# Optimization experiments

Hardware: AMD Instinct MI355X
Metric: run time of the kernel (lower is better)

Reference implementation:

```python
import jax, jax.numpy as jnp
import numpy as np

D, H, DFF = 1024, 16, 4096
HD = D // H
NEG = -1e9  # finite stand-in for -inf causal mask (grad-safe)


def layer_norm(x, g, b, eps=1e-5):
    mu = jnp.mean(x, axis=-1, keepdims=True)
    var = jnp.mean(jnp.square(x - mu), axis=-1, keepdims=True)
    return (x - mu) * jax.lax.rsqrt(var + eps) * g + b


def setup_inputs() -> dict:
    key = jax.random.key(0)
    ks = jax.random.split(key, 16)
    B, T = 2, 2048
    x = jax.random.normal(ks[0], (B, T, D), jnp.float32)
    causal_mask = jnp.where(jnp.triu(jnp.ones((T, T), bool), k=1), NEG, 0.0).astype(jnp.float32)
    ema_attn = jax.random.uniform(ks[1], (H, T, T), jnp.float32)
    # normalize EMA rows like attention weights would be
    ema_attn = ema_attn / jnp.sum(ema_attn, axis=-1, keepdims=True)
    s = 0.02
    p = {
        'x': x, 'causal_mask': causal_mask, 'ema_attn': ema_attn,
        'log_tau_attn': jnp.array(0.0, jnp.float32),
        'Wq': jax.random.normal(ks[2], (D, D), jnp.float32) * s,
        'bq': jnp.zeros((D,), jnp.float32),
        'Wk': jax.random.normal(ks[3], (D, D), jnp.float32) * s,
        'bk': jnp.zeros((D,), jnp.float32),
        'Wv': jax.random.normal(ks[4], (D, D), jnp.float32) * s,
        'bv': jnp.zeros((D,), jnp.float32),
        'Wo': jax.random.normal(ks[5], (D, D), jnp.float32) * s,
        'bo': jnp.zeros((D,), jnp.float32),
        'W1': jax.random.normal(ks[6], (DFF, D), jnp.float32) * s,
        'b1': jnp.zeros((DFF,), jnp.float32),
        'W2': jax.random.normal(ks[7], (D, DFF), jnp.float32) * s,
        'b2': jnp.zeros((D,), jnp.float32),
        'g1': jnp.ones((D,), jnp.float32), 'beta1': jnp.zeros((D,), jnp.float32),
        'g2': jnp.ones((D,), jnp.float32), 'beta2': jnp.zeros((D,), jnp.float32),
    }
    return p


def reference(x, causal_mask, ema_attn, log_tau_attn, Wq, bq, Wk, bk, Wv, bv,
              Wo, bo, W1, b1, W2, b2, g1, beta1, g2, beta2):
    B, T, _ = x.shape
    # habituation bias: -tau_a * mean over heads of the EMA attention
    tau_a = jnp.exp(log_tau_attn)
    habit_bias = -(tau_a * ema_attn).mean(0)            # (T, T)
    attn_mask = causal_mask + habit_bias                # (T, T)

    # multi-head self-attention (torch MHA math, dropout=0 / eval)
    q = (x @ Wq.T + bq).reshape(B, T, H, HD)
    k = (x @ Wk.T + bk).reshape(B, T, H, HD)
    v = (x @ Wv.T + bv).reshape(B, T, H, HD)
    scores = jnp.einsum('bthd,bshd->bhts', q, k) / jnp.sqrt(jnp.float32(HD))
    scores = scores + attn_mask[None, None]             # (B, H, T, T)
    attn = jax.nn.softmax(scores, axis=-1)
    ctx = jnp.einsum('bhts,bshd->bthd', attn, v).reshape(B, T, D)
    attn_out = ctx @ Wo.T + bo

    # residual + norm, then FFN (GELU), residual + norm
    h = layer_norm(x + attn_out, g1, beta1)
    ff = (jax.nn.gelu(h @ W1.T + b1) @ W2.T) + b2
    out = layer_norm(h + ff, g2, beta2)
    return out
```

## Files before the change

### kernel.cpp

```cpp
#include <hip/hip_runtime.h>
#include <hip/hip_bf16.h>
#include <math.h>

#define T_SEQ 2048
#define D_MODEL 1024
#define BT 4096

typedef __bf16 bf16;
typedef __bf16 bf16x8 __attribute__((ext_vector_type(8)));
typedef __bf16 bf16x4 __attribute__((ext_vector_type(4)));
typedef float f32x4 __attribute__((ext_vector_type(4)));

__device__ __forceinline__ void gload_lds16(const bf16* g, bf16* l) {
  __builtin_amdgcn_global_load_lds(
      (__attribute__((address_space(1))) void*)(g),
      (__attribute__((address_space(3))) void*)(l), 16, 0, 0);
}

__global__ __launch_bounds__(256) void k_mask(const float* __restrict__ causal,
                                              const float* __restrict__ ema,
                                              const float* __restrict__ logtau,
                                              bf16* __restrict__ mask) {
  const int qt = blockIdx.x, st = blockIdx.y;
  if (st > qt) return;
  const int t = threadIdx.x;
  const float c = -__expf(logtau[0]) * (1.0f / 16.0f);
  const int r0 = t >> 4;
  const int cc = t & 15;
#pragma unroll
  for (int rr = 0; rr < 4; ++rr) {
    const size_t q = (size_t)qt * 64 + r0 + rr * 16;
    const size_t f4 = q * 512 + st * 16 + cc;
    float4 v = ((const float4*)causal)[f4];
    float a0 = v.x, a1 = v.y, a2 = v.z, a3 = v.w;
#pragma unroll
    for (int h = 0; h < 16; ++h) {
      float4 e = ((const float4*)(ema + (size_t)h * T_SEQ * T_SEQ))[f4];
      a0 += c * e.x; a1 += c * e.y; a2 += c * e.z; a3 += c * e.w;
    }
    bf16x4 o;
    o[0] = (bf16)a0; o[1] = (bf16)a1; o[2] = (bf16)a2; o[3] = (bf16)a3;
    ((bf16x4*)mask)[f4] = o;
  }
}

struct CvtArgs {
  const float* src[7];
  bf16* dst[7];
  int cum[8];
};
__global__ __launch_bounds__(256) void k_cvt_all(CvtArgs a) {
  const int i = blockIdx.x * 256 + threadIdx.x;
  if (i >= a.cum[7]) return;
  int s = 0;
#pragma unroll
  for (int k = 1; k < 7; ++k) s += (i >= a.cum[k]);
  const int j = i - a.cum[s];
  float4 v = ((const float4*)a.src[s])[j];
  bf16x4 o;
  o[0] = (bf16)v.x; o[1] = (bf16)v.y; o[2] = (bf16)v.z; o[3] = (bf16)v.w;
  ((bf16x4*)a.dst[s])[j] = o;
}

__global__ void k_bias3(const float* __restrict__ bq, const float* __restrict__ bk,
                        const float* __restrict__ bv, float* __restrict__ o) {
  const int i = blockIdx.x * 256 + threadIdx.x;
  o[i] = (i < 1024) ? bq[i] : (i < 2048 ? bk[i - 1024] : bv[i - 2048]);
}

__device__ __forceinline__ float gelu_tanh(float x) {
  return 0.5f * x * (1.0f + tanhf(0.7978845608028654f * (x + 0.044715f * x * x * x)));
}

template <int EPI>
__global__ __launch_bounds__(512, 2) void k_gemm_big(const bf16* __restrict__ A,
                                                     const bf16* __restrict__ B,
                                                     const float* __restrict__ bias,
                                                     const float* __restrict__ resid,
                                                     float* __restrict__ outf,
                                                     bf16* __restrict__ outb,
                                                     int K, int N) {
  __shared__ bf16 sA[2][256 * 64];
  __shared__ bf16 sB[2][256 * 64];
  const int tid = threadIdx.x;
  const int m0 = blockIdx.x * 256, n0 = blockIdx.y * 256;
  const int lane = tid & 63;
  const int w = tid >> 6, wr = w >> 2, wc = w & 3;
  const int lr = lane & 15, lg = lane >> 4;

  const int srow = lane >> 3;
  const int schunk = (lane & 7) ^ srow;

  auto stage = [&](int buf, int kt) {
    const int k0 = kt << 6;
#pragma unroll
    for (int e = 0; e < 4; ++e) {
      const int r = w * 32 + e * 8 + srow;
      gload_lds16(A + (size_t)(m0 + r) * K + k0 + schunk * 8,
                  &sA[buf][(w * 32 + e * 8) * 64 + lane * 8]);
      gload_lds16(B + (size_t)(n0 + r) * K + k0 + schunk * 8,
                  &sB[buf][(w * 32 + e * 8) * 64 + lane * 8]);
    }
  };

  f32x4 acc[8][4] = {};

  stage(0, 0);
  stage(1, 1);

  const int KT = K >> 6;
  for (int t = 0; t < KT; ++t) {
    if (t < KT - 1) asm volatile("s_waitcnt vmcnt(8)" ::: "memory");
    else            asm volatile("s_waitcnt vmcnt(0)" ::: "memory");
    __builtin_amdgcn_s_barrier();

    const int buf = t & 1;
    const char* pA = (const char*)sA[buf];
    const char* pB = (const char*)sB[buf];

    bf16x8 a0[8], b0[4];
#pragma unroll
    for (int m = 0; m < 8; ++m) {
      const int row = wr * 128 + m * 16 + lr;
      a0[m] = *(const bf16x8*)(pA + (unsigned)(row * 128) +
                               (((unsigned)lg) ^ (unsigned)(row & 7)) * 16u);
    }
#pragma unroll
    for (int n = 0; n < 4; ++n) {
      const int row = wc * 64 + n * 16 + lr;
      b0[n] = *(const bf16x8*)(pB + (unsigned)(row * 128) +
                               (((unsigned)lg) ^ (unsigned)(row & 7)) * 16u);
    }
    __builtin_amdgcn_s_setprio(1);
#pragma unroll
    for (int m = 0; m < 8; ++m)
#pragma unroll
      for (int n = 0; n < 4; ++n)
        acc[m][n] = __builtin_amdgcn_mfma_f32_16x16x32_bf16(a0[m], b0[n], acc[m][n], 0, 0, 0);
    __builtin_amdgcn_s_setprio(0);

    bf16x8 a1[8], b1[4];
#pragma unroll
    for (int m = 0; m < 8; ++m) {
      const int row = wr * 128 + m * 16 + lr;
      a1[m] = *(const bf16x8*)(pA + (unsigned)(row * 128) +
                               (((unsigned)(4 | lg)) ^ (unsigned)(row & 7)) * 16u);
    }
#pragma unroll
    for (int n = 0; n < 4; ++n) {
      const int row = wc * 64 + n * 16 + lr;
      b1[n] = *(const bf16x8*)(pB + (unsigned)(row * 128) +
                               (((unsigned)(4 | lg)) ^ (unsigned)(row & 7)) * 16u);
    }
    asm volatile("s_waitcnt lgkmcnt(0)" ::: "memory");
    __builtin_amdgcn_s_barrier();
    if (t + 2 < KT) stage(buf, t + 2);

    __builtin_amdgcn_s_setprio(1);
#pragma unroll
    for (int m = 0; m < 8; ++m)
#pragma unroll
      for (int n = 0; n < 4; ++n)
        acc[m][n] = __builtin_amdgcn_mfma_f32_16x16x32_bf16(a1[m], b1[n], acc[m][n], 0, 0, 0);
    __builtin_amdgcn_s_setprio(0);
  }

  const int row0 = m0 + wr * 128 + (lane >> 4) * 4;
  const int col0 = n0 + wc * 64 + lr;
#pragma unroll
  for (int m = 0; m < 8; ++m) {
#pragma unroll
    for (int n = 0; n < 4; ++n) {
      const int col = col0 + n * 16;
      const float bv = bias[col];
#pragma unroll
      for (int r = 0; r < 4; ++r) {
        const int row = row0 + m * 16 + r;
        float v = acc[m][n][r] + bv;
        if (EPI == 0) {
          outb[(size_t)row * N + col] = (bf16)v;
        } else if (EPI == 1) {
          v += resid[(size_t)row * N + col];
          outf[(size_t)row * N + col] = v;
        } else {
          outb[(size_t)row * N + col] = (bf16)gelu_tanh(v);
        }
      }
    }
  }
}

__global__ __launch_bounds__(256, 2) void k_gemm_splitk(const bf16* __restrict__ A,
                                                        const bf16* __restrict__ B,
                                                        const float* __restrict__ bias,
                                                        float* __restrict__ p0,
                                                        float* __restrict__ p1,
                                                        int K, int N, int Kc) {
  __shared__ bf16 sA[2][128 * 64];
  __shared__ bf16 sB[2][128 * 64];
  const int tid = threadIdx.x;
  const int m0 = blockIdx.x * 128, n0 = blockIdx.y * 128;
  const int z = blockIdx.z;
  const int kb = z * Kc;
  float* __restrict__ po = z ? p1 : p0;
  const int lane = tid & 63;
  const int w = tid >> 6, wr = w >> 1, wc = w & 1;
  const int lr = lane & 15, lg = lane >> 4;

  const int srow = lane >> 3;
  const int schunk = (lane & 7) ^ srow;

  auto stage = [&](int buf, int kt) {
    const int k0 = kb + (kt << 6);
#pragma unroll
    for (int e = 0; e < 4; ++e) {
      const int r = w * 32 + e * 8 + srow;
      gload_lds16(A + (size_t)(m0 + r) * K + k0 + schunk * 8,
                  &sA[buf][(w * 32 + e * 8) * 64 + lane * 8]);
      gload_lds16(B + (size_t)(n0 + r) * K + k0 + schunk * 8,
                  &sB[buf][(w * 32 + e * 8) * 64 + lane * 8]);
    }
  };

  f32x4 acc[4][4] = {};

  stage(0, 0);
  stage(1, 1);

  const int KT = Kc >> 6;
  for (int t = 0; t < KT; ++t) {
    if (t < KT - 1) asm volatile("s_waitcnt vmcnt(8)" ::: "memory");
    else            asm volatile("s_waitcnt vmcnt(0)" ::: "memory");
    __builtin_amdgcn_s_barrier();

    const int buf = t & 1;
    const char* pA = (const char*)sA[buf];
    const char* pB = (const char*)sB[buf];
    bf16x8 af[4][2], bfr[4][2];
#pragma unroll
    for (int m = 0; m < 4; ++m) {
      const int row = wr * 64 + m * 16 + lr;
#pragma unroll
      for (int kk = 0; kk < 2; ++kk) {
        const unsigned off =
            (unsigned)(row * 128) + (((unsigned)((kk << 2) | lg)) ^ (unsigned)(row & 7)) * 16u;
        af[m][kk] = *(const bf16x8*)(pA + off);
      }
    }
#pragma unroll
    for (int n = 0; n < 4; ++n) {
      const int row = wc * 64 + n * 16 + lr;
#pragma unroll
      for (int kk = 0; kk < 2; ++kk) {
        const unsigned off =
            (unsigned)(row * 128) + (((unsigned)((kk << 2) | lg)) ^ (unsigned)(row & 7)) * 16u;
        bfr[n][kk] = *(const bf16x8*)(pB + off);
      }
    }
    asm volatile("s_waitcnt lgkmcnt(0)" ::: "memory");
    __builtin_amdgcn_s_barrier();
    if (t + 2 < KT) stage(buf, t + 2);

    __builtin_amdgcn_s_setprio(1);
#pragma unroll
    for (int m = 0; m < 4; ++m)
#pragma unroll
      for (int n = 0; n < 4; ++n)
#pragma unroll
        for (int kk = 0; kk < 2; ++kk)
          acc[m][n] = __builtin_amdgcn_mfma_f32_16x16x32_bf16(af[m][kk], bfr[n][kk],
                                                              acc[m][n], 0, 0, 0);
    __builtin_amdgcn_s_setprio(0);
  }

  const int row0 = m0 + wr * 64 + (lane >> 4) * 4;
  const int col0 = n0 + wc * 64 + lr;
#pragma unroll
  for (int m = 0; m < 4; ++m) {
#pragma unroll
    for (int n = 0; n < 4; ++n) {
      const int col = col0 + n * 16;
      const float bv = z ? 0.0f : bias[col];
#pragma unroll
      for (int r = 0; r < 4; ++r) {
        const int row = row0 + m * 16 + r;
        po[(size_t)row * N + col] = acc[m][n][r] + bv;
      }
    }
  }
}

__global__ __launch_bounds__(256, 3) void k_attn(const bf16* __restrict__ qkv,
                                                 const bf16* __restrict__ maskb,
                                                 bf16* __restrict__ ctx) {
  const int bh = blockIdx.x;
  const int qt = blockIdx.y;
  const int b = bh >> 4, h = bh & 15;
  const int tid = threadIdx.x, w = tid >> 6, lane = tid & 63;
  const int lr = lane & 15, lg = lane >> 4;

  __shared__ bf16 sK[2][64 * 64];
  __shared__ bf16 sVt[2][64 * 72];
  __shared__ bf16 sP[4][16 * 64];

  const size_t rs = 3072;
  const bf16* base = qkv + (size_t)b * T_SEQ * rs + h * 64;
  const int q0b = qt * 64;
  const int qrow = w * 16 + lr;
  const bf16* mrow = maskb + (size_t)(q0b + qrow) * T_SEQ;

  bf16x8 qf[2];
#pragma unroll
  for (int kk = 0; kk < 2; ++kk) {
    bf16x8 q = *(const bf16x8*)(base + (size_t)(q0b + qrow) * rs + kk * 32 + lg * 8);
#pragma unroll
    for (int j = 0; j < 8; ++j) qf[kk][j] = (bf16)((float)q[j] * 0.125f);
  }

  const int srow = lane >> 3;
  const int scol = lane & 7;

  auto issueK = [&](int s0, bf16* sKb) {
#pragma unroll
    for (int e = 0; e < 2; ++e) {
      const int kb = w * 16 + e * 8;
      const int r = kb + srow;
      const int cs = 8 * (scol ^ (r & 7));
      gload_lds16(base + (size_t)(s0 + r) * rs + 1024 + cs, &sKb[kb * 64 + lane * 8]);
    }
  };
  auto loadV = [&](int s0, bf16x8 vv[2]) {
#pragma unroll
    for (int t = 0; t < 2; ++t) {
      const int c = w * 64 + lane + t * 256;
      vv[t] = *(const bf16x8*)(base + (size_t)(s0 + (c >> 3)) * rs + 2048 + (c & 7) * 8);
    }
  };
  auto writeV = [&](const bf16x8 vv[2], bf16* sVtb) {
    char* pb = (char*)sVtb;
#pragma unroll
    for (int t = 0; t < 2; ++t) {
      const int c = w * 64 + lane + t * 256;
      const int s = c >> 3, dc = c & 7;
#pragma unroll
      for (int j = 0; j < 8; ++j) {
        const unsigned ba = ((unsigned)((dc * 8 + j) * 72 + s) * 2) ^ ((unsigned)dc << 4);
        *(bf16*)(pb + ba) = vv[t][j];
      }
    }
  };

  float m_r = -3.0e38f, l_r = 0.0f;
  f32x4 o[4] = {};

  const float L2E = 1.44269504088896f;
  const int nt = qt + 1;
  const unsigned swzq = (unsigned)(lr & 7) << 4;

  {
    bf16x8 v0[2];
    loadV(0, v0);
    issueK(0, sK[0]);
    writeV(v0, sVt[0]);
  }
  __syncthreads();

  int cur = 0;
  for (int t = 0; t < nt; ++t, cur ^= 1) {
    const bool pf = (t + 1 < nt);
    bf16x8 vv[2];
    if (pf) {
      loadV((t + 1) * 64, vv);
      issueK((t + 1) * 64, sK[cur ^ 1]);
    }

    bf16x4 mk[4];
#pragma unroll
    for (int n = 0; n < 4; ++n)
      mk[n] = *(const bf16x4*)(mrow + t * 64 + n * 16 + lg * 4);

    const char* sKc = (const char*)sK[cur];
    f32x4 sc[4] = {};
    __builtin_amdgcn_s_setprio(1);
#pragma unroll
    for (int n = 0; n < 4; ++n) {
      const int key = n * 16 + lr;
#pragma unroll
      for (int kk = 0; kk < 2; ++kk) {
        const unsigned boff =
            (unsigned)(key * 128 + kk * 64 + lg * 16) ^ ((unsigned)(key & 7) << 4);
        bf16x8 kf = *(const bf16x8*)(sKc + boff);
        sc[n] = __builtin_amdgcn_mfma_f32_16x16x32_bf16(kf, qf[kk], sc[n], 0, 0, 0);
      }
    }
    __builtin_amdgcn_s_setprio(0);

    float mx = -3.0e38f;
#pragma unroll
    for (int n = 0; n < 4; ++n)
#pragma unroll
      for (int j = 0; j < 4; ++j) {
        sc[n][j] += (float)mk[n][j];
        mx = fmaxf(mx, sc[n][j]);
      }
    mx = fmaxf(mx, __shfl_xor(mx, 16));
    mx = fmaxf(mx, __shfl_xor(mx, 32));

    if (!__all(mx <= m_r + 8.0f)) {
      const float mnew = fmaxf(m_r, mx);
      const float alpha = exp2f((m_r - mnew) * L2E);
      m_r = mnew;
      l_r *= alpha;
      float a4[4];
#pragma unroll
      for (int j = 0; j < 4; ++j) a4[j] = __shfl(alpha, (lane & 48) | (lg * 4 + j));
#pragma unroll
      for (int dt = 0; dt < 4; ++dt)
#pragma unroll
        for (int j = 0; j < 4; ++j) o[dt][j] *= a4[j];
    }

    const float mL2 = m_r * L2E;
    float ps = 0.0f;
    float pn[4][4];
#pragma unroll
    for (int n = 0; n < 4; ++n)
#pragma unroll
      for (int j = 0; j < 4; ++j) {
        const float p = exp2f(sc[n][j] * L2E - mL2);
        pn[n][j] = p;
        ps += p;
      }
    ps += __shfl_xor(ps, 16);
    ps += __shfl_xor(ps, 32);
    l_r += ps;

    if (pf) writeV(vv, sVt[cur ^ 1]);

    char* sPw = (char*)sP[w];
#pragma unroll
    for (int n = 0; n < 4; ++n) {
      bf16x4 pb;
#pragma unroll
      for (int j = 0; j < 4; ++j) pb[j] = (bf16)pn[n][j];
      *(bf16x4*)(sPw + (((unsigned)(lr * 128 + n * 32 + lg * 8)) ^ swzq)) = pb;
    }

    bf16x8 pa[2];
#pragma unroll
    for (int kk = 0; kk < 2; ++kk)
      pa[kk] = *(const bf16x8*)(sPw + (((unsigned)(lr * 128 + kk * 64 + lg * 16)) ^ swzq));
    const char* sVc = (const char*)sVt[cur];
    __builtin_amdgcn_s_setprio(1);
#pragma unroll
    for (int dt = 0; dt < 4; ++dt) {
      const int dd = dt * 16 + lr;
#pragma unroll
      for (int kk = 0; kk < 2; ++kk) {
        const unsigned ba =
            ((unsigned)(dd * 72 + kk * 32 + lg * 8) * 2) ^ ((unsigned)((dd >> 3) & 7) << 4);
        bf16x8 vb = *(const bf16x8*)(sVc + ba);
        o[dt] = __builtin_amdgcn_mfma_f32_16x16x32_bf16(pa[kk], vb, o[dt], 0, 0, 0);
      }
    }
    __builtin_amdgcn_s_setprio(0);
    __syncthreads();
  }

  float linv[4];
#pragma unroll
  for (int j = 0; j < 4; ++j) linv[j] = 1.0f / __shfl(l_r, (lane & 48) | (lg * 4 + j));
#pragma unroll
  for (int j = 0; j < 4; ++j) {
    const size_t row = (size_t)b * T_SEQ + q0b + w * 16 + lg * 4 + j;
#pragma unroll
    for (int dt = 0; dt < 4; ++dt)
      ctx[row * D_MODEL + h * 64 + dt * 16 + lr] = (bf16)(o[dt][j] * linv[j]);
  }
}

__global__ __launch_bounds__(256) void k_ln3(const float* __restrict__ p0,
                                             const float* __restrict__ p1,
                                             const float* __restrict__ resid,
                                             const float* __restrict__ g,
                                             const float* __restrict__ be,
                                             float* __restrict__ out,
                                             bf16* __restrict__ outb) {
  const int row = blockIdx.x, tid = threadIdx.x;
  const size_t i4 = (size_t)row * 256 + tid;
  const float4 a = ((const float4*)p0)[i4];
  const float4 bq = ((const float4*)p1)[i4];
  const float4 cr = ((const float4*)resid)[i4];
  float4 v;
  v.x = a.x + bq.x + cr.x;
  v.y = a.y + bq.y + cr.y;
  v.z = a.z + bq.z + cr.z;
  v.w = a.w + bq.w + cr.w;
  float s = v.x + v.y + v.z + v.w;
  float s2 = v.x * v.x + v.y * v.y + v.z * v.z + v.w * v.w;
#pragma unroll
  for (int d = 1; d < 64; d <<= 1) { s += __shfl_xor(s, d); s2 += __shfl_xor(s2, d); }
  __shared__ float red[8];
  const int w = tid >> 6;
  if ((tid & 63) == 0) { red[w] = s; red[4 + w] = s2; }
  __syncthreads();
  s = red[0] + red[1] + red[2] + red[3];
  s2 = red[4] + red[5] + red[6] + red[7];
  const float mu = s * (1.0f / 1024.0f);
  const float var = s2 * (1.0f / 1024.0f) - mu * mu;
  const float inv = rsqrtf(var + 1e-5f);
  const int col = tid * 4;
  const float4 gv = *(const float4*)(g + col);
  const float4 bv = *(const float4*)(be + col);
  float4 y;
  y.x = (v.x - mu) * inv * gv.x + bv.x;
  y.y = (v.y - mu) * inv * gv.y + bv.y;
  y.z = (v.z - mu) * inv * gv.z + bv.z;
  y.w = (v.w - mu) * inv * gv.w + bv.w;
  *(float4*)(out + (size_t)row * 1024 + col) = y;
  if (outb) {
    bf16x4 ob;
    ob[0] = (bf16)y.x; ob[1] = (bf16)y.y; ob[2] = (bf16)y.z; ob[3] = (bf16)y.w;
    *(bf16x4*)(outb + (size_t)row * 1024 + col) = ob;
  }
}

extern "C" void kernel_launch(void* const* d_in, const int* in_sizes, int n_in,
                              void* d_out, int out_size, void* d_ws, size_t ws_size,
                              hipStream_t stream) {
  const float* x      = (const float*)d_in[0];
  const float* causal = (const float*)d_in[1];
  const float* ema    = (const float*)d_in[2];
  const float* logtau = (const float*)d_in[3];
  const float* Wq = (const float*)d_in[4];
  const float* bq = (const float*)d_in[5];
  const float* Wk = (const float*)d_in[6];
  const float* bk = (const float*)d_in[7];
  const float* Wv = (const float*)d_in[8];
  const float* bv = (const float*)d_in[9];
  const float* Wo = (const float*)d_in[10];
  const float* bo = (const float*)d_in[11];
  const float* W1 = (const float*)d_in[12];
  const float* b1 = (const float*)d_in[13];
  const float* W2 = (const float*)d_in[14];
  const float* b2 = (const float*)d_in[15];
  const float* g1  = (const float*)d_in[16];
  const float* be1 = (const float*)d_in[17];
  const float* g2  = (const float*)d_in[18];
  const float* be2 = (const float*)d_in[19];
  float* out = (float*)d_out;

  char* ws = (char*)d_ws;
  bf16*  maskb = (bf16*)(ws + 0);
  bf16*  x_bf  = (bf16*)(ws + (16UL << 20));
  bf16*  wqkv  = (bf16*)(ws + (24UL << 20));
  bf16*  wo_bf = (bf16*)(ws + (30UL << 20));
  bf16*  w1_bf = (bf16*)(ws + (32UL << 20));
  bf16*  w2_bf = (bf16*)(ws + (40UL << 20));
  float* bqkv  = (float*)(ws + (48UL << 20));
  bf16*  qkv   = (bf16*)(ws + (49UL << 20));
  bf16*  ctxb  = (bf16*)(ws + (73UL << 20));
  float* hbuf  = (float*)(ws + (97UL << 20));
  bf16*  h_bf  = (bf16*)(ws + (113UL << 20));
  bf16*  ff1   = (bf16*)(ws + (121UL << 20));
  float* part0 = (float*)(ws + (49UL << 20));
  float* part1 = (float*)(ws + 0);

  const dim3 blk(256);
  const dim3 blk512(512);

  k_mask<<<dim3(32, 32), blk, 0, stream>>>(causal, ema, logtau, maskb);

  CvtArgs ca;
  ca.src[0] = x;  ca.dst[0] = x_bf;
  ca.src[1] = Wq; ca.dst[1] = wqkv;
  ca.src[2] = Wk; ca.dst[2] = wqkv + (1UL << 20);
  ca.src[3] = Wv; ca.dst[3] = wqkv + (2UL << 20);
  ca.src[4] = Wo; ca.dst[4] = wo_bf;
  ca.src[5] = W1; ca.dst[5] = w1_bf;
  ca.src[6] = W2; ca.dst[6] = w2_bf;
  ca.cum[0] = 0;
  ca.cum[1] = 1048576;
  ca.cum[2] = 1048576 + 262144;
  ca.cum[3] = 1048576 + 524288;
  ca.cum[4] = 1048576 + 786432;
  ca.cum[5] = 2097152;
  ca.cum[6] = 2097152 + 1048576;
  ca.cum[7] = 4194304;
  k_cvt_all<<<dim3(16384), blk, 0, stream>>>(ca);
  k_bias3<<<dim3(12), blk, 0, stream>>>(bq, bk, bv, bqkv);

  k_gemm_big<0><<<dim3(16, 12), blk512, 0, stream>>>(x_bf, wqkv, bqkv, nullptr, nullptr,
                                                     qkv, 1024, 3072);

  k_attn<<<dim3(32, 32), blk, 0, stream>>>(qkv, maskb, ctxb);

  k_gemm_splitk<<<dim3(32, 8, 2), blk, 0, stream>>>(ctxb, wo_bf, bo, part0, part1,
                                                    1024, 1024, 512);

  k_ln3<<<dim3(4096), blk, 0, stream>>>(part0, part1, x, g1, be1, hbuf, h_bf);

  k_gemm_big<2><<<dim3(16, 16), blk512, 0, stream>>>(h_bf, w1_bf, b1, nullptr, nullptr,
                                                     ff1, 1024, 4096);

  k_gemm_splitk<<<dim3(32, 8, 2), blk, 0, stream>>>(ff1, w2_bf, b2, part0, part1,
                                                    4096, 1024, 2048);

  k_ln3<<<dim3(4096), blk, 0, stream>>>(part0, part1, hbuf, g2, be2, out, nullptr);
}
```

Measured before the change: 304.2 us.

## Widen attention blocks to 128 query rows with 8 waves sharing K/V tiles

The attention kernel now processes 128 query rows per block using 8 waves (512 threads), so each K/V tile loaded into LDS is shared by twice as many query rows. This halves the per-query K/V traffic and the block count. Blocks are also remapped so the y index pairs short and long causal rows, giving heavy tiles first. The mask kernel now fills one extra key tile beyond the diagonal, because the 128-row blocks walk a key range that extends past it. The costs are more LDS per block, lower occupancy, and a diagonal tile that does masked work.

```diff
diff --git a/kernel.cpp b/kernel.cpp
--- a/kernel.cpp
+++ b/kernel.cpp
@@ -22,7 +22,7 @@
                                               const float* __restrict__ logtau,
                                               bf16* __restrict__ mask) {
   const int qt = blockIdx.x, st = blockIdx.y;
-  if (st > qt) return;
+  if (st > qt + 1) return;
   const int t = threadIdx.x;
   const float c = -__expf(logtau[0]) * (1.0f / 16.0f);
   const int r0 = t >> 4;
@@ -290,22 +290,23 @@
   }
 }
 
-__global__ __launch_bounds__(256, 3) void k_attn(const bf16* __restrict__ qkv,
+__global__ __launch_bounds__(512, 4) void k_attn(const bf16* __restrict__ qkv,
                                                  const bf16* __restrict__ maskb,
                                                  bf16* __restrict__ ctx) {
   const int bh = blockIdx.x;
-  const int qt = blockIdx.y;
+  const int y = blockIdx.y;
+  const int qt2 = (y < 8) ? y : 23 - y;
   const int b = bh >> 4, h = bh & 15;
   const int tid = threadIdx.x, w = tid >> 6, lane = tid & 63;
   const int lr = lane & 15, lg = lane >> 4;
 
   __shared__ bf16 sK[2][64 * 64];
   __shared__ bf16 sVt[2][64 * 72];
-  __shared__ bf16 sP[4][16 * 64];
+  __shared__ bf16 sP[8][16 * 64];
 
   const size_t rs = 3072;
   const bf16* base = qkv + (size_t)b * T_SEQ * rs + h * 64;
-  const int q0b = qt * 64;
+  const int q0b = qt2 * 128;
   const int qrow = w * 16 + lr;
   const bf16* mrow = maskb + (size_t)(q0b + qrow) * T_SEQ;
 
@@ -321,32 +322,21 @@
   const int scol = lane & 7;
 
   auto issueK = [&](int s0, bf16* sKb) {
-#pragma unroll
-    for (int e = 0; e < 2; ++e) {
-      const int kb = w * 16 + e * 8;
-      const int r = kb + srow;
-      const int cs = 8 * (scol ^ (r & 7));
-      gload_lds16(base + (size_t)(s0 + r) * rs + 1024 + cs, &sKb[kb * 64 + lane * 8]);
-    }
+    const int kb = w * 8;
+    const int r = kb + srow;
+    const int cs = 8 * (scol ^ (r & 7));
+    gload_lds16(base + (size_t)(s0 + r) * rs + 1024 + cs, &sKb[kb * 64 + lane * 8]);
   };
-  auto loadV = [&](int s0, bf16x8 vv[2]) {
-#pragma unroll
-    for (int t = 0; t < 2; ++t) {
-      const int c = w * 64 + lane + t * 256;
-      vv[t] = *(const bf16x8*)(base + (size_t)(s0 + (c >> 3)) * rs + 2048 + (c & 7) * 8);
-    }
+  auto loadV = [&](int s0, bf16x8& vv) {
+    vv = *(const bf16x8*)(base + (size_t)(s0 + (tid >> 3)) * rs + 2048 + (tid & 7) * 8);
   };
-  auto writeV = [&](const bf16x8 vv[2], bf16* sVtb) {
+  auto writeV = [&](const bf16x8& vv, bf16* sVtb) {
     char* pb = (char*)sVtb;
-#pragma unroll
-    for (int t = 0; t < 2; ++t) {
-      const int c = w * 64 + lane + t * 256;
-      const int s = c >> 3, dc = c & 7;
-#pragma unroll
-      for (int j = 0; j < 8; ++j) {
-        const unsigned ba = ((unsigned)((dc * 8 + j) * 72 + s) * 2) ^ ((unsigned)dc << 4);
-        *(bf16*)(pb + ba) = vv[t][j];
-      }
+    const int s = tid >> 3, dc = tid & 7;
+#pragma unroll
+    for (int j = 0; j < 8; ++j) {
+      const unsigned ba = ((unsigned)((dc * 8 + j) * 72 + s) * 2) ^ ((unsigned)dc << 4);
+      *(bf16*)(pb + ba) = vv[j];
     }
   };
 
@@ -354,11 +344,11 @@
   f32x4 o[4] = {};
 
   const float L2E = 1.44269504088896f;
-  const int nt = qt + 1;
+  const int nt = 2 * qt2 + 2;
   const unsigned swzq = (unsigned)(lr & 7) << 4;
 
   {
-    bf16x8 v0[2];
+    bf16x8 v0;
     loadV(0, v0);
     issueK(0, sK[0]);
     writeV(v0, sVt[0]);
@@ -368,7 +358,7 @@
   int cur = 0;
   for (int t = 0; t < nt; ++t, cur ^= 1) {
     const bool pf = (t + 1 < nt);
-    bf16x8 vv[2];
+    bf16x8 vv;
     if (pf) {
       loadV((t + 1) * 64, vv);
       issueK((t + 1) * 64, sK[cur ^ 1]);
@@ -593,7 +583,7 @@
   k_gemm_big<0><<<dim3(16, 12), blk512, 0, stream>>>(x_bf, wqkv, bqkv, nullptr, nullptr,
                                                      qkv, 1024, 3072);
 
-  k_attn<<<dim3(32, 32), blk, 0, stream>>>(qkv, maskb, ctxb);
+  k_attn<<<dim3(32, 16), blk512, 0, stream>>>(qkv, maskb, ctxb);
 
   k_gemm_splitk<<<dim3(32, 8, 2), blk, 0, stream>>>(ctxb, wo_bf, bo, part0, part1,
                                                     1024, 1024, 512);
```

Measured after the change: 298.2 us. No clear change (-2.0%).

## Double attention query tile per block to reuse K/V tiles across two row groups

Applied to the files above, without the earlier changes.

Each attention block now covers 128 query rows instead of 64, with each wave handling two 16-row groups that share the same K and V fragments loaded from LDS. The query-tile index is remapped so heavy and light causal tiles are paired for load balance, and the mask kernel now fills one extra diagonal tile because key tiles extend past the 64-row diagonal. This halves K/V global and LDS traffic per query row and cuts the block count. In exchange it raises register use (occupancy hint lowered from 3 to 2) and gives fewer, longer blocks.

```diff
diff --git a/kernel.cpp b/kernel.cpp
--- a/kernel.cpp
+++ b/kernel.cpp
@@ -22,7 +22,7 @@
                                               const float* __restrict__ logtau,
                                               bf16* __restrict__ mask) {
   const int qt = blockIdx.x, st = blockIdx.y;
-  if (st > qt) return;
+  if (st > qt + 1) return;
   const int t = threadIdx.x;
   const float c = -__expf(logtau[0]) * (1.0f / 16.0f);
   const int r0 = t >> 4;
@@ -290,32 +290,36 @@
   }
 }
 
-__global__ __launch_bounds__(256, 3) void k_attn(const bf16* __restrict__ qkv,
+__global__ __launch_bounds__(256, 2) void k_attn(const bf16* __restrict__ qkv,
                                                  const bf16* __restrict__ maskb,
                                                  bf16* __restrict__ ctx) {
   const int bh = blockIdx.x;
-  const int qt = blockIdx.y;
+  const int y = blockIdx.y;
+  const int qt2 = (y < 8) ? y : 23 - y;
   const int b = bh >> 4, h = bh & 15;
   const int tid = threadIdx.x, w = tid >> 6, lane = tid & 63;
   const int lr = lane & 15, lg = lane >> 4;
 
   __shared__ bf16 sK[2][64 * 64];
   __shared__ bf16 sVt[2][64 * 72];
-  __shared__ bf16 sP[4][16 * 64];
+  __shared__ bf16 sP[4][32 * 64];
 
   const size_t rs = 3072;
   const bf16* base = qkv + (size_t)b * T_SEQ * rs + h * 64;
-  const int q0b = qt * 64;
-  const int qrow = w * 16 + lr;
-  const bf16* mrow = maskb + (size_t)(q0b + qrow) * T_SEQ;
-
-  bf16x8 qf[2];
-#pragma unroll
-  for (int kk = 0; kk < 2; ++kk) {
-    bf16x8 q = *(const bf16x8*)(base + (size_t)(q0b + qrow) * rs + kk * 32 + lg * 8);
-#pragma unroll
-    for (int j = 0; j < 8; ++j) qf[kk][j] = (bf16)((float)q[j] * 0.125f);
-  }
+  const int q0b = qt2 * 128;
+  const bf16* mrow0 = maskb + (size_t)(q0b + w * 32 + lr) * T_SEQ;
+  const bf16* mrow1 = mrow0 + (size_t)16 * T_SEQ;
+
+  bf16x8 qf[2][2];
+#pragma unroll
+  for (int qr = 0; qr < 2; ++qr)
+#pragma unroll
+    for (int kk = 0; kk < 2; ++kk) {
+      bf16x8 q = *(const bf16x8*)(base + (size_t)(q0b + w * 32 + qr * 16 + lr) * rs +
+                                  kk * 32 + lg * 8);
+#pragma unroll
+      for (int j = 0; j < 8; ++j) qf[qr][kk][j] = (bf16)((float)q[j] * 0.125f);
+    }
 
   const int srow = lane >> 3;
   const int scol = lane & 7;
@@ -350,11 +354,11 @@
     }
   };
 
-  float m_r = -3.0e38f, l_r = 0.0f;
-  f32x4 o[4] = {};
+  float m_r[2] = {-3.0e38f, -3.0e38f}, l_r[2] = {0.0f, 0.0f};
+  f32x4 o[2][4] = {};
 
   const float L2E = 1.44269504088896f;
-  const int nt = qt + 1;
+  const int nt = 2 * qt2 + 2;
   const unsigned swzq = (unsigned)(lr & 7) << 4;
 
   {
@@ -374,14 +378,15 @@
       issueK((t + 1) * 64, sK[cur ^ 1]);
     }
 
-    bf16x4 mk[4];
-#pragma unroll
-    for (int n = 0; n < 4; ++n)
-      mk[n] = *(const bf16x4*)(mrow + t * 64 + n * 16 + lg * 4);
+    bf16x4 mk[2][4];
+#pragma unroll
+    for (int n = 0; n < 4; ++n) {
+      mk[0][n] = *(const bf16x4*)(mrow0 + t * 64 + n * 16 + lg * 4);
+      mk[1][n] = *(const bf16x4*)(mrow1 + t * 64 + n * 16 + lg * 4);
+    }
 
     const char* sKc = (const char*)sK[cur];
-    f32x4 sc[4] = {};
-    __builtin_amdgcn_s_setprio(1);
+    bf16x8 kf[4][2];
 #pragma unroll
     for (int n = 0; n < 4; ++n) {
       const int key = n * 16 + lr;
@@ -389,69 +394,81 @@
       for (int kk = 0; kk < 2; ++kk) {
         const unsigned boff =
             (unsigned)(key * 128 + kk * 64 + lg * 16) ^ ((unsigned)(key & 7) << 4);
-        bf16x8 kf = *(const bf16x8*)(sKc + boff);
-        sc[n] = __builtin_amdgcn_mfma_f32_16x16x32_bf16(kf, qf[kk], sc[n], 0, 0, 0);
-      }
-    }
+        kf[n][kk] = *(const bf16x8*)(sKc + boff);
+      }
+    }
+
+    f32x4 sc[2][4] = {};
+    __builtin_amdgcn_s_setprio(1);
+#pragma unroll
+    for (int qr = 0; qr < 2; ++qr)
+#pragma unroll
+      for (int n = 0; n < 4; ++n)
+#pragma unroll
+        for (int kk = 0; kk < 2; ++kk)
+          sc[qr][n] = __builtin_amdgcn_mfma_f32_16x16x32_bf16(kf[n][kk], qf[qr][kk],
+                                                              sc[qr][n], 0, 0, 0);
     __builtin_amdgcn_s_setprio(0);
 
-    float mx = -3.0e38f;
-#pragma unroll
-    for (int n = 0; n < 4; ++n)
-#pragma unroll
-      for (int j = 0; j < 4; ++j) {
-        sc[n][j] += (float)mk[n][j];
-        mx = fmaxf(mx, sc[n][j]);
-      }
-    mx = fmaxf(mx, __shfl_xor(mx, 16));
-    mx = fmaxf(mx, __shfl_xor(mx, 32));
-
-    if (!__all(mx <= m_r + 8.0f)) {
-      const float mnew = fmaxf(m_r, mx);
-      const float alpha = exp2f((m_r - mnew) * L2E);
-      m_r = mnew;
-      l_r *= alpha;
-      float a4[4];
-#pragma unroll
-      for (int j = 0; j < 4; ++j) a4[j] = __shfl(alpha, (lane & 48) | (lg * 4 + j));
-#pragma unroll
-      for (int dt = 0; dt < 4; ++dt)
-#pragma unroll
-        for (int j = 0; j < 4; ++j) o[dt][j] *= a4[j];
-    }
-
-    const float mL2 = m_r * L2E;
-    float ps = 0.0f;
-    float pn[4][4];
-#pragma unroll
-    for (int n = 0; n < 4; ++n)
-#pragma unroll
-      for (int j = 0; j < 4; ++j) {
-        const float p = exp2f(sc[n][j] * L2E - mL2);
-        pn[n][j] = p;
-        ps += p;
-      }
-    ps += __shfl_xor(ps, 16);
-    ps += __shfl_xor(ps, 32);
-    l_r += ps;
+    float pn[2][4][4];
+#pragma unroll
+    for (int qr = 0; qr < 2; ++qr) {
+      float mx = -3.0e38f;
+#pragma unroll
+      for (int n = 0; n < 4; ++n)
+#pragma unroll
+        for (int j = 0; j < 4; ++j) {
+          sc[qr][n][j] += (float)mk[qr][n][j];
+          mx = fmaxf(mx, sc[qr][n][j]);
+        }
+      mx = fmaxf(mx, __shfl_xor(mx, 16));
+      mx = fmaxf(mx, __shfl_xor(mx, 32));
+
+      if (!__all(mx <= m_r[qr] + 8.0f)) {
+        const float mnew = fmaxf(m_r[qr], mx);
+        const float alpha = exp2f((m_r[qr] - mnew) * L2E);
+        m_r[qr] = mnew;
+        l_r[qr] *= alpha;
+        float a4[4];
+#pragma unroll
+        for (int j = 0; j < 4; ++j) a4[j] = __shfl(alpha, (lane & 48) | (lg * 4 + j));
+#pragma unroll
+        for (int dt = 0; dt < 4; ++dt)
+#pragma unroll
+          for (int j = 0; j < 4; ++j) o[qr][dt][j] *= a4[j];
+      }
+
+      const float mL2 = m_r[qr] * L2E;
+      float ps = 0.0f;
+#pragma unroll
+      for (int n = 0; n < 4; ++n)
+#pragma unroll
+        for (int j = 0; j < 4; ++j) {
+          const float p = exp2f(sc[qr][n][j] * L2E - mL2);
+          pn[qr][n][j] = p;
+          ps += p;
+        }
+      ps += __shfl_xor(ps, 16);
+      ps += __shfl_xor(ps, 32);
+      l_r[qr] += ps;
+    }
 
     if (pf) writeV(vv, sVt[cur ^ 1]);
 
     char* sPw = (char*)sP[w];
 #pragma unroll
-    for (int n = 0; n < 4; ++n) {
-      bf16x4 pb;
-#pragma unroll
-      for (int j = 0; j < 4; ++j) pb[j] = (bf16)pn[n][j];
-      *(bf16x4*)(sPw + (((unsigned)(lr * 128 + n * 32 + lg * 8)) ^ swzq)) = pb;
-    }
-
-    bf16x8 pa[2];
-#pragma unroll
-    for (int kk = 0; kk < 2; ++kk)
-      pa[kk] = *(const bf16x8*)(sPw + (((unsigned)(lr * 128 + kk * 64 + lg * 16)) ^ swzq));
+    for (int qr = 0; qr < 2; ++qr)
+#pragma unroll
+      for (int n = 0; n < 4; ++n) {
+        bf16x4 pb;
+#pragma unroll
+        for (int j = 0; j < 4; ++j) pb[j] = (bf16)pn[qr][n][j];
+        *(bf16x4*)(sPw + qr * 2048 +
+                   (((unsigned)(lr * 128 + n * 32 + lg * 8)) ^ swzq)) = pb;
+      }
+
     const char* sVc = (const char*)sVt[cur];
-    __builtin_amdgcn_s_setprio(1);
+    bf16x8 vb[4][2];
 #pragma unroll
     for (int dt = 0; dt < 4; ++dt) {
       const int dd = dt * 16 + lr;
@@ -459,23 +476,42 @@
       for (int kk = 0; kk < 2; ++kk) {
         const unsigned ba =
             ((unsigned)(dd * 72 + kk * 32 + lg * 8) * 2) ^ ((unsigned)((dd >> 3) & 7) << 4);
-        bf16x8 vb = *(const bf16x8*)(sVc + ba);
-        o[dt] = __builtin_amdgcn_mfma_f32_16x16x32_bf16(pa[kk], vb, o[dt], 0, 0, 0);
-      }
+        vb[dt][kk] = *(const bf16x8*)(sVc + ba);
+      }
+    }
+
+    __builtin_amdgcn_s_setprio(1);
+#pragma unroll
+    for (int qr = 0; qr < 2; ++qr) {
+      bf16x8 pa[2];
+#pragma unroll
+      for (int kk = 0; kk < 2; ++kk)
+        pa[kk] = *(const bf16x8*)(sPw + qr * 2048 +
+                                  (((unsigned)(lr * 128 + kk * 64 + lg * 16)) ^ swzq));
+#pragma unroll
+      for (int dt = 0; dt < 4; ++dt)
+#pragma unroll
+        for (int kk = 0; kk < 2; ++kk)
+          o[qr][dt] = __builtin_amdgcn_mfma_f32_16x16x32_bf16(pa[kk], vb[dt][kk],
+                                                              o[qr][dt], 0, 0, 0);
     }
     __builtin_amdgcn_s_setprio(0);
     __syncthreads();
   }
 
-  float linv[4];
-#pragma unroll
-  for (int j = 0; j < 4; ++j) linv[j] = 1.0f / __shfl(l_r, (lane & 48) | (lg * 4 + j));
-#pragma unroll
-  for (int j = 0; j < 4; ++j) {
-    const size_t row = (size_t)b * T_SEQ + q0b + w * 16 + lg * 4 + j;
-#pragma unroll
-    for (int dt = 0; dt < 4; ++dt)
-      ctx[row * D_MODEL + h * 64 + dt * 16 + lr] = (bf16)(o[dt][j] * linv[j]);
+#pragma unroll
+  for (int qr = 0; qr < 2; ++qr) {
+    float linv[4];
+#pragma unroll
+    for (int j = 0; j < 4; ++j)
+      linv[j] = 1.0f / __shfl(l_r[qr], (lane & 48) | (lg * 4 + j));
+#pragma unroll
+    for (int j = 0; j < 4; ++j) {
+      const size_t row = (size_t)b * T_SEQ + q0b + w * 32 + qr * 16 + lg * 4 + j;
+#pragma unroll
+      for (int dt = 0; dt < 4; ++dt)
+        ctx[row * D_MODEL + h * 64 + dt * 16 + lr] = (bf16)(o[qr][dt][j] * linv[j]);
+    }
   }
 }
 
@@ -593,7 +629,7 @@
   k_gemm_big<0><<<dim3(16, 12), blk512, 0, stream>>>(x_bf, wqkv, bqkv, nullptr, nullptr,
                                                      qkv, 1024, 3072);
 
-  k_attn<<<dim3(32, 32), blk, 0, stream>>>(qkv, maskb, ctxb);
+  k_attn<<<dim3(32, 16), blk, 0, stream>>>(qkv, maskb, ctxb);
 
   k_gemm_splitk<<<dim3(32, 8, 2), blk, 0, stream>>>(ctxb, wo_bf, bo, part0, part1,
                                                     1024, 1024, 512);
```

Result: no change. 306.9 us (+0.9%).
